# Performance work log

Measured on AMD Instinct MI355X. Metric: run time of the kernel, lower is better.

The kernel has to match this reference:

```python
import jax, jax.numpy as jnp
import numpy as np

ATTEN = 2  # window half-size -> 2*ATTEN+1 = 5 neighbors
B, S, IN, H, MID, OUT = 1024, 100, 100, 128, 32, 2
MAX_LEN = 100
SQRT_H = float(np.sqrt(float(H)))


def _xavier(k, i, o):
    return jax.random.normal(k, (i, o), jnp.float32) * np.sqrt(2.0 / (i + o))


def _positional_encoding():
    pos = np.arange(MAX_LEN, dtype=np.float32)[:, None]
    div = np.exp(np.arange(0, H, 2, dtype=np.float32) * (-np.log(10000.0) / H))
    pe = np.zeros((MAX_LEN, H), np.float32)
    pe[:, 0::2] = np.sin(pos * div)
    pe[:, 1::2] = np.cos(pos * div)
    return jnp.asarray(pe[None])  # (1, MAX_LEN, H)


def setup_inputs() -> dict:
    key = jax.random.key(0)
    ks = jax.random.split(key, 7)
    return {
        "x": jax.random.normal(ks[0], (B, S, IN), jnp.float32),
        "W1": _xavier(ks[1], IN, H),
        "b1": jnp.zeros((1, 1, H), jnp.float32),
        "Wq": _xavier(ks[2], H, H),
        "Wk": _xavier(ks[3], H, H),
        "Wv": _xavier(ks[4], H, H),
        "bv": jnp.zeros((1, 1, H), jnp.float32),
        "W2": _xavier(ks[5], H, MID),
        "b2": jnp.zeros((1, 1, MID), jnp.float32),
        "W3": _xavier(ks[6], MID, OUT),
        "b3": jnp.zeros((1, 1, OUT), jnp.float32),
        "pe": _positional_encoding(),
    }


def reference(x, W1, b1, Wq, Wk, Wv, bv, W2, b2, W3, b3, pe):
    seq_len = x.shape[1]
    h = jax.nn.relu(x @ W1 + b1) + pe[:, :seq_len, :]  # (B,S,H)
    # zero-pad seq dim by ATTEN on each side; torch pad+roll+stack+slice is
    # equivalent to gathering window offsets +2,+1,0,-1,-2 (in that order)
    padded = jnp.pad(h, ((0, 0), (ATTEN, ATTEN), (0, 0)))
    x_nei = jnp.stack(
        [padded[:, ATTEN - k: ATTEN - k + seq_len, :] for k in range(-ATTEN, ATTEN + 1)],
        axis=2,
    )  # (B,S,5,H); index m corresponds to neighbor x[i + ATTEN - m]
    q = h @ Wq                      # (B,S,H)
    keys = x_nei @ Wk               # (B,S,5,H)
    vals = x_nei @ Wv + bv          # (B,S,5,H)
    scores = jnp.einsum("bsh,bswh->bsw", q, keys) / SQRT_H
    w = jax.nn.softmax(scores, axis=-1)  # (B,S,5)
    context = jnp.einsum("bsw,bswh->bsh", w, vals)
    output = jax.nn.relu(context @ W2 + b2) @ W3 + b3  # (B,S,OUT)
    return output, w[:, :, None, :]  # weights shaped (B,S,1,5) like torch
```

## Files before the change

### kernel.cpp

```cpp
#include <hip/hip_runtime.h>
#include <hip/hip_bf16.h>

#define B_ 1024
#define S_ 100
#define IN_ 100
#define H_ 128
#define MID_ 32
#define OUT_ 2
#define P_ (B_ * S_)
#define RSQRT_H 0.08838834764831845f
#define LSTR 136
#define MROWS 100

typedef __attribute__((ext_vector_type(8))) short short8;
typedef __attribute__((ext_vector_type(4))) short short4v;
typedef __attribute__((ext_vector_type(4))) float float4v;

__device__ __forceinline__ float bf2f(ushort u) {
    union { unsigned u; float f; } c; c.u = ((unsigned)u) << 16; return c.f;
}
__device__ __forceinline__ ushort f2bf(float x) {
    union { float f; unsigned u; } c; c.f = x;
    unsigned r = c.u + 0x7FFFu + ((c.u >> 16) & 1u);
    return (ushort)(r >> 16);
}

__global__ __launch_bounds__(256) void prep_kernel(
    const float* __restrict__ W1, const float* __restrict__ Wv,
    const float* __restrict__ W2, const float* __restrict__ Wq,
    const float* __restrict__ Wk,
    ushort* __restrict__ W1T, ushort* __restrict__ WvT,
    ushort* __restrict__ W2T, ushort* __restrict__ WqkT) {
    int tid = threadIdx.x;
    if (blockIdx.x < 144) {
        int g = blockIdx.x * 256 + tid;
        if (g < 16384) {
            int n = g >> 7, k = g & 127;
            W1T[g] = (k < IN_) ? f2bf(W1[k * H_ + n]) : (ushort)0;
        } else if (g < 32768) {
            int e = g - 16384; int n = e >> 7, k = e & 127;
            WvT[e] = f2bf(Wv[k * H_ + n]);
        } else {
            int e = g - 32768; int n = e >> 7, k = e & 127;
            W2T[e] = f2bf(W2[k * MID_ + n]);
        }
    } else {
        __shared__ float sq[32][132];
        __shared__ float sk[32][132];
        int bid = blockIdx.x - 144;
        int n0 = (bid >> 2) * 32, k0 = (bid & 3) * 32;
        for (int i = tid; i < 32 * 32; i += 256) {
            int r = i >> 5, c4 = (i & 31) * 4;
            float4 a = *(const float4*)(Wq + (k0 + r) * H_ + c4);
            float4 b = *(const float4*)(Wk + (n0 + r) * H_ + c4);
            sq[r][c4] = a.x; sq[r][c4 + 1] = a.y; sq[r][c4 + 2] = a.z; sq[r][c4 + 3] = a.w;
            sk[r][c4] = b.x; sk[r][c4 + 1] = b.y; sk[r][c4 + 2] = b.z; sk[r][c4 + 3] = b.w;
        }
        __syncthreads();
        for (int i = tid; i < 1024; i += 256) {
            int kk = i & 31, nn = i >> 5;
            float a0 = 0.f, a1 = 0.f, a2 = 0.f, a3 = 0.f;
#pragma unroll
            for (int j = 0; j < 128; j += 4) {
                a0 += sq[kk][j + 0] * sk[nn][j + 0];
                a1 += sq[kk][j + 1] * sk[nn][j + 1];
                a2 += sq[kk][j + 2] * sk[nn][j + 2];
                a3 += sq[kk][j + 3] * sk[nn][j + 3];
            }
            WqkT[(n0 + nn) * 128 + (k0 + kk)] = f2bf((a0 + a1) + (a2 + a3));
        }
    }
}

template <int EPI>
__device__ __forceinline__ void mm_stage(const ushort* __restrict__ A_lds,
                                         const ushort* __restrict__ WT,
                                         ushort* __restrict__ C_lds,
                                         int wave, int lane,
                                         const float* __restrict__ bias,
                                         const float* __restrict__ pe) {
    int l15 = lane & 15, quad = lane >> 4;
    int n = wave * 16 + l15;
    short8 bfrag[4];
#pragma unroll
    for (int ks = 0; ks < 4; ++ks)
        bfrag[ks] = *(const short8*)(WT + n * 128 + ks * 32 + quad * 8);
    float biasv = 0.f;
    if (EPI != 0) biasv = bias[n];
#pragma unroll
    for (int mt = 0; mt < 7; ++mt) {
        int m0 = (mt < 6) ? mt * 16 : 84;
        short8 afrag[4];
#pragma unroll
        for (int ks = 0; ks < 4; ++ks)
            afrag[ks] = *(const short8*)(A_lds + (m0 + l15) * LSTR + ks * 32 + quad * 8);
        float4v acc = {0.f, 0.f, 0.f, 0.f};
#pragma unroll
        for (int ks = 0; ks < 4; ++ks)
            acc = __builtin_amdgcn_mfma_f32_16x16x32_bf16(afrag[ks], bfrag[ks], acc, 0, 0, 0);
#pragma unroll
        for (int i = 0; i < 4; ++i) {
            int row = m0 + quad * 4 + i;
            float v = acc[i];
            if (EPI == 1) v = fmaxf(v + biasv, 0.f) + pe[row * H_ + n];
            else if (EPI == 2) v = v + biasv;
            C_lds[row * LSTR + n] = f2bf(v);
        }
    }
}

__global__ __launch_bounds__(512, 4) void fused_kernel(
    const float* __restrict__ x, const ushort* __restrict__ W1T,
    const ushort* __restrict__ WqkT, const ushort* __restrict__ WvT,
    const ushort* __restrict__ W2T,
    const float* __restrict__ b1, const float* __restrict__ bv,
    const float* __restrict__ b2, const float* __restrict__ W3,
    const float* __restrict__ b3, const float* __restrict__ pe,
    float* __restrict__ out, float* __restrict__ wout) {
    __shared__ ushort klds[MROWS * LSTR];
    __shared__ ushort xh[MROWS * LSTR];
    int tid = threadIdx.x, wave = tid >> 6, lane = tid & 63;
    int b = blockIdx.x;
    const float* xb = x + (size_t)b * (S_ * IN_);

    for (int i = tid; i < 2500; i += 512) {
        float4 v = ((const float4*)xb)[i];
        int m = i / 25, k4 = (i - m * 25) * 4;
        short4v s;
        s[0] = (short)f2bf(v.x); s[1] = (short)f2bf(v.y);
        s[2] = (short)f2bf(v.z); s[3] = (short)f2bf(v.w);
        *(short4v*)(klds + m * LSTR + k4) = s;
    }
    for (int i = tid; i < S_ * 28; i += 512) {
        int r = i / 28, c = i - r * 28;
        klds[r * LSTR + 100 + c] = 0;
    }
    __syncthreads();
    mm_stage<1>(klds, W1T, xh, wave, lane, b1, pe);
    __syncthreads();
    mm_stage<0>(xh, WqkT, klds, wave, lane, nullptr, nullptr);
    __syncthreads();
    if (tid < 4 * S_) {
        int r = tid >> 2, q = tid & 3;
        const ushort* kqr = klds + r * LSTR + q * 32;
        float kqf[32];
#pragma unroll
        for (int c = 0; c < 4; ++c) {
            short8 v = *(const short8*)(kqr + c * 8);
#pragma unroll
            for (int j = 0; j < 8; ++j) kqf[c * 8 + j] = bf2f((ushort)v[j]);
        }
        float sc[5];
#pragma unroll
        for (int m = 0; m < 5; ++m) {
            int nr = r + 2 - m;
            float p = 0.f;
            if (nr >= 0 && nr < S_) {
                const ushort* hr = xh + nr * LSTR + q * 32;
#pragma unroll
                for (int c = 0; c < 4; ++c) {
                    short8 v = *(const short8*)(hr + c * 8);
#pragma unroll
                    for (int j = 0; j < 8; ++j) p += bf2f((ushort)v[j]) * kqf[c * 8 + j];
                }
            }
            sc[m] = p;
        }
#pragma unroll
        for (int m = 0; m < 5; ++m) {
            sc[m] += __shfl_xor(sc[m], 1);
            sc[m] += __shfl_xor(sc[m], 2);
            sc[m] *= RSQRT_H;
        }
        float mx = sc[0];
#pragma unroll
        for (int m = 1; m < 5; ++m) mx = fmaxf(mx, sc[m]);
        float e[5], ss = 0.f;
#pragma unroll
        for (int m = 0; m < 5; ++m) { e[m] = expf(sc[m] - mx); ss += e[m]; }
        float inv = 1.f / ss;
        float w5[5];
#pragma unroll
        for (int m = 0; m < 5; ++m) w5[m] = e[m] * inv;
        if (q == 0) {
            float* wp = wout + (size_t)b * (S_ * 5) + r * 5;
#pragma unroll
            for (int m = 0; m < 5; ++m) wp[m] = w5[m];
        }
        float acc[32];
#pragma unroll
        for (int c = 0; c < 32; ++c) acc[c] = 0.f;
#pragma unroll
        for (int m = 0; m < 5; ++m) {
            int nr = r + 2 - m;
            if (nr < 0 || nr >= S_) continue;
            float wm = w5[m];
            const ushort* hr = xh + nr * LSTR + q * 32;
#pragma unroll
            for (int c = 0; c < 4; ++c) {
                short8 v = *(const short8*)(hr + c * 8);
#pragma unroll
                for (int j = 0; j < 8; ++j) acc[c * 8 + j] += wm * bf2f((ushort)v[j]);
            }
        }
        ushort* op = klds + r * LSTR + q * 32;
#pragma unroll
        for (int c = 0; c < 4; ++c) {
            short8 v;
#pragma unroll
            for (int j = 0; j < 8; ++j) v[j] = (short)f2bf(acc[c * 8 + j]);
            *(short8*)(op + c * 8) = v;
        }
    }
    __syncthreads();
    mm_stage<2>(klds, WvT, xh, wave, lane, bv, nullptr);
    __syncthreads();
    {
        int l15 = lane & 15, quad = lane >> 4;
        for (int t = wave; t < 14; t += 8) {
            int mt = t >> 1, nt = t & 1;
            int m0 = (mt < 6) ? mt * 16 : 84;
            short8 bfrag[4];
#pragma unroll
            for (int ks = 0; ks < 4; ++ks)
                bfrag[ks] = *(const short8*)(W2T + (nt * 16 + l15) * 128 + ks * 32 + quad * 8);
            float biasv = b2[nt * 16 + l15];
            short8 afrag[4];
#pragma unroll
            for (int ks = 0; ks < 4; ++ks)
                afrag[ks] = *(const short8*)(xh + (m0 + l15) * LSTR + ks * 32 + quad * 8);
            float4v acc = {0.f, 0.f, 0.f, 0.f};
#pragma unroll
            for (int ks = 0; ks < 4; ++ks)
                acc = __builtin_amdgcn_mfma_f32_16x16x32_bf16(afrag[ks], bfrag[ks], acc, 0, 0, 0);
#pragma unroll
            for (int i = 0; i < 4; ++i) {
                int row = m0 + quad * 4 + i;
                klds[row * LSTR + nt * 16 + l15] = f2bf(fmaxf(acc[i] + biasv, 0.f));
            }
        }
    }
    __syncthreads();
    if (tid < S_) {
        int r = tid;
        float o0 = b3[0], o1 = b3[1];
#pragma unroll
        for (int k = 0; k < MID_; ++k) {
            float mv = bf2f(klds[r * LSTR + k]);
            o0 += mv * W3[k * 2];
            o1 += mv * W3[k * 2 + 1];
        }
        float* op = out + (size_t)b * (S_ * OUT_) + r * OUT_;
        op[0] = o0; op[1] = o1;
    }
}

extern "C" void kernel_launch(void* const* d_in, const int* in_sizes, int n_in,
                              void* d_out, int out_size, void* d_ws, size_t ws_size,
                              hipStream_t stream) {
    const float* x  = (const float*)d_in[0];
    const float* W1 = (const float*)d_in[1];
    const float* b1 = (const float*)d_in[2];
    const float* Wq = (const float*)d_in[3];
    const float* Wk = (const float*)d_in[4];
    const float* Wv = (const float*)d_in[5];
    const float* bv = (const float*)d_in[6];
    const float* W2 = (const float*)d_in[7];
    const float* b2 = (const float*)d_in[8];
    const float* W3 = (const float*)d_in[9];
    const float* b3 = (const float*)d_in[10];
    const float* pe = (const float*)d_in[11];

    float* out  = (float*)d_out;
    float* wout = out + (size_t)P_ * OUT_;

    ushort* W1T  = (ushort*)d_ws;
    ushort* WqkT = W1T + 16384;
    ushort* WvT  = WqkT + 16384;
    ushort* W2T  = WvT + 16384;

    prep_kernel<<<160, 256, 0, stream>>>(W1, Wv, W2, Wq, Wk, W1T, WvT, W2T, WqkT);
    fused_kernel<<<B_, 512, 0, stream>>>(x, W1T, WqkT, WvT, W2T,
                                         b1, bv, b2, W3, b3, pe, out, wout);
}
```

Measured before the change: 135.3 us.

## Move local attention scores and context onto MFMA via banded GEMMs

```diff
diff --git a/kernel.cpp b/kernel.cpp
--- a/kernel.cpp
+++ b/kernel.cpp
@@ -10,7 +10,11 @@
 #define P_ (B_ * S_)
 #define RSQRT_H 0.08838834764831845f
 #define LSTR 136
-#define MROWS 100
+#define HSTR 136
+
+#define R1_OFF 13600
+#define R2_OFF 27200
+#define POOL_SHORTS (27200 + 17408)
 
 typedef __attribute__((ext_vector_type(8))) short short8;
 typedef __attribute__((ext_vector_type(4))) short short4v;
@@ -23,6 +27,24 @@
     union { float f; unsigned u; } c; c.f = x;
     unsigned r = c.u + 0x7FFFu + ((c.u >> 16) & 1u);
     return (ushort)(r >> 16);
+}
+
+__device__ const int BAND_M0[19] = {0,0,16,16,16,32,32,32,48,48,48,64,64,64,80,80,80,84,84};
+__device__ const int BAND_N0[19] = {0,16,0,16,32,16,32,48,32,48,64,48,64,80,64,80,84,80,84};
+
+__device__ __forceinline__ float4v gemm_task(const ushort* A, int astr,
+                                             const ushort* Bt, int bstr,
+                                             int m0, int n0, int ks0, int ks1,
+                                             int l15, int quad) {
+    float4v acc = {0.f, 0.f, 0.f, 0.f};
+    const ushort* ap = A + (m0 + l15) * astr + quad * 8;
+    const ushort* bp = Bt + (n0 + l15) * bstr + quad * 8;
+    for (int ks = ks0; ks <= ks1; ++ks) {
+        short8 a = *(const short8*)(ap + ks * 32);
+        short8 b = *(const short8*)(bp + ks * 32);
+        acc = __builtin_amdgcn_mfma_f32_16x16x32_bf16(a, b, acc, 0, 0, 0);
+    }
+    return acc;
 }
 
 __global__ __launch_bounds__(256) void prep_kernel(
@@ -72,44 +94,7 @@
     }
 }
 
-template <int EPI>
-__device__ __forceinline__ void mm_stage(const ushort* __restrict__ A_lds,
-                                         const ushort* __restrict__ WT,
-                                         ushort* __restrict__ C_lds,
-                                         int wave, int lane,
-                                         const float* __restrict__ bias,
-                                         const float* __restrict__ pe) {
-    int l15 = lane & 15, quad = lane >> 4;
-    int n = wave * 16 + l15;
-    short8 bfrag[4];
-#pragma unroll
-    for (int ks = 0; ks < 4; ++ks)
-        bfrag[ks] = *(const short8*)(WT + n * 128 + ks * 32 + quad * 8);
-    float biasv = 0.f;
-    if (EPI != 0) biasv = bias[n];
-#pragma unroll
-    for (int mt = 0; mt < 7; ++mt) {
-        int m0 = (mt < 6) ? mt * 16 : 84;
-        short8 afrag[4];
-#pragma unroll
-        for (int ks = 0; ks < 4; ++ks)
-            afrag[ks] = *(const short8*)(A_lds + (m0 + l15) * LSTR + ks * 32 + quad * 8);
-        float4v acc = {0.f, 0.f, 0.f, 0.f};
-#pragma unroll
-        for (int ks = 0; ks < 4; ++ks)
-            acc = __builtin_amdgcn_mfma_f32_16x16x32_bf16(afrag[ks], bfrag[ks], acc, 0, 0, 0);
-#pragma unroll
-        for (int i = 0; i < 4; ++i) {
-            int row = m0 + quad * 4 + i;
-            float v = acc[i];
-            if (EPI == 1) v = fmaxf(v + biasv, 0.f) + pe[row * H_ + n];
-            else if (EPI == 2) v = v + biasv;
-            C_lds[row * LSTR + n] = f2bf(v);
-        }
-    }
-}
-
-__global__ __launch_bounds__(512, 4) void fused_kernel(
+__global__ __launch_bounds__(1024, 4) void fused_kernel(
     const float* __restrict__ x, const ushort* __restrict__ W1T,
     const ushort* __restrict__ WqkT, const ushort* __restrict__ WvT,
     const ushort* __restrict__ W2T,
@@ -117,138 +102,151 @@
     const float* __restrict__ b2, const float* __restrict__ W3,
     const float* __restrict__ b3, const float* __restrict__ pe,
     float* __restrict__ out, float* __restrict__ wout) {
-    __shared__ ushort klds[MROWS * LSTR];
-    __shared__ ushort xh[MROWS * LSTR];
+    __shared__ __align__(16) ushort pool[POOL_SHORTS];
+    ushort* R0 = pool;
+    ushort* R1 = pool + R1_OFF;
+    ushort* R2 = pool + R2_OFF;
+    float* scf = (float*)R2;
+
     int tid = threadIdx.x, wave = tid >> 6, lane = tid & 63;
+    int l15 = lane & 15, quad = lane >> 4;
     int b = blockIdx.x;
     const float* xb = x + (size_t)b * (S_ * IN_);
 
-    for (int i = tid; i < 2500; i += 512) {
+    for (int i = tid; i < 2500; i += 1024) {
         float4 v = ((const float4*)xb)[i];
         int m = i / 25, k4 = (i - m * 25) * 4;
         short4v s;
         s[0] = (short)f2bf(v.x); s[1] = (short)f2bf(v.y);
         s[2] = (short)f2bf(v.z); s[3] = (short)f2bf(v.w);
-        *(short4v*)(klds + m * LSTR + k4) = s;
-    }
-    for (int i = tid; i < S_ * 28; i += 512) {
+        *(short4v*)(R0 + m * LSTR + k4) = s;
+    }
+    for (int i = tid; i < S_ * 28; i += 1024) {
         int r = i / 28, c = i - r * 28;
-        klds[r * LSTR + 100 + c] = 0;
-    }
-    __syncthreads();
-    mm_stage<1>(klds, W1T, xh, wave, lane, b1, pe);
-    __syncthreads();
-    mm_stage<0>(xh, WqkT, klds, wave, lane, nullptr, nullptr);
-    __syncthreads();
-    if (tid < 4 * S_) {
-        int r = tid >> 2, q = tid & 3;
-        const ushort* kqr = klds + r * LSTR + q * 32;
-        float kqf[32];
-#pragma unroll
-        for (int c = 0; c < 4; ++c) {
-            short8 v = *(const short8*)(kqr + c * 8);
-#pragma unroll
-            for (int j = 0; j < 8; ++j) kqf[c * 8 + j] = bf2f((ushort)v[j]);
-        }
-        float sc[5];
+        R0[r * LSTR + 100 + c] = 0;
+    }
+    if (tid < 800) scf[tid] = 0.f;
+    __syncthreads();
+
+    for (int t = wave; t < 56; t += 16) {
+        int mt = t >> 3, nt = t & 7;
+        int m0 = (mt < 6) ? mt * 16 : 84, n0 = nt * 16;
+        float4v acc = gemm_task(R0, LSTR, W1T, 128, m0, n0, 0, 3, l15, quad);
+        int n = n0 + l15;
+        float bb = b1[n];
+#pragma unroll
+        for (int i = 0; i < 4; ++i) {
+            int row = m0 + quad * 4 + i;
+            R1[row * LSTR + n] = f2bf(fmaxf(acc[i] + bb, 0.f) + pe[row * H_ + n]);
+        }
+    }
+    __syncthreads();
+
+    for (int t = wave; t < 56; t += 16) {
+        int mt = t >> 3, nt = t & 7;
+        int m0 = (mt < 6) ? mt * 16 : 84, n0 = nt * 16;
+        float4v acc = gemm_task(R1, LSTR, WqkT, 128, m0, n0, 0, 3, l15, quad);
+        int n = n0 + l15;
+#pragma unroll
+        for (int i = 0; i < 4; ++i)
+            R0[(m0 + quad * 4 + i) * LSTR + n] = f2bf(acc[i]);
+    }
+    __syncthreads();
+
+    for (int t = wave; t < 19; t += 16) {
+        int m0 = BAND_M0[t], n0 = BAND_N0[t];
+        float4v acc = gemm_task(R0, LSTR, R1, LSTR, m0, n0, 0, 3, l15, quad);
+        int col = n0 + l15;
+#pragma unroll
+        for (int i = 0; i < 4; ++i) {
+            int row = m0 + quad * 4 + i;
+            int m = row - col + 2;
+            if ((unsigned)m <= 4u) scf[row * 8 + m] = acc[i];
+        }
+    }
+    __syncthreads();
+
+    {
+        short8 z = {0, 0, 0, 0, 0, 0, 0, 0};
+        for (int i = tid; i < 1600; i += 1024)
+            *(short8*)(R0 + (i >> 4) * LSTR + (i & 15) * 8) = z;
+    }
+    __syncthreads();
+    if (tid < S_) {
+        int r = tid;
+        float sc5[5];
+#pragma unroll
+        for (int m = 0; m < 5; ++m) sc5[m] = scf[r * 8 + m] * RSQRT_H;
+        float mx = fmaxf(fmaxf(fmaxf(sc5[0], sc5[1]), fmaxf(sc5[2], sc5[3])), sc5[4]);
+        float e[5], ss = 0.f;
+#pragma unroll
+        for (int m = 0; m < 5; ++m) { e[m] = expf(sc5[m] - mx); ss += e[m]; }
+        float inv = 1.f / ss;
+        float* wp = wout + (size_t)b * (S_ * 5) + r * 5;
 #pragma unroll
         for (int m = 0; m < 5; ++m) {
-            int nr = r + 2 - m;
-            float p = 0.f;
-            if (nr >= 0 && nr < S_) {
-                const ushort* hr = xh + nr * LSTR + q * 32;
-#pragma unroll
-                for (int c = 0; c < 4; ++c) {
-                    short8 v = *(const short8*)(hr + c * 8);
-#pragma unroll
-                    for (int j = 0; j < 8; ++j) p += bf2f((ushort)v[j]) * kqf[c * 8 + j];
-                }
-            }
-            sc[m] = p;
-        }
-#pragma unroll
-        for (int m = 0; m < 5; ++m) {
-            sc[m] += __shfl_xor(sc[m], 1);
-            sc[m] += __shfl_xor(sc[m], 2);
-            sc[m] *= RSQRT_H;
-        }
-        float mx = sc[0];
-#pragma unroll
-        for (int m = 1; m < 5; ++m) mx = fmaxf(mx, sc[m]);
-        float e[5], ss = 0.f;
-#pragma unroll
-        for (int m = 0; m < 5; ++m) { e[m] = expf(sc[m] - mx); ss += e[m]; }
-        float inv = 1.f / ss;
-        float w5[5];
-#pragma unroll
-        for (int m = 0; m < 5; ++m) w5[m] = e[m] * inv;
-        if (q == 0) {
-            float* wp = wout + (size_t)b * (S_ * 5) + r * 5;
-#pragma unroll
-            for (int m = 0; m < 5; ++m) wp[m] = w5[m];
-        }
-        float acc[32];
-#pragma unroll
-        for (int c = 0; c < 32; ++c) acc[c] = 0.f;
-#pragma unroll
-        for (int m = 0; m < 5; ++m) {
-            int nr = r + 2 - m;
-            if (nr < 0 || nr >= S_) continue;
-            float wm = w5[m];
-            const ushort* hr = xh + nr * LSTR + q * 32;
-#pragma unroll
-            for (int c = 0; c < 4; ++c) {
-                short8 v = *(const short8*)(hr + c * 8);
-#pragma unroll
-                for (int j = 0; j < 8; ++j) acc[c * 8 + j] += wm * bf2f((ushort)v[j]);
-            }
-        }
-        ushort* op = klds + r * LSTR + q * 32;
-#pragma unroll
-        for (int c = 0; c < 4; ++c) {
-            short8 v;
-#pragma unroll
-            for (int j = 0; j < 8; ++j) v[j] = (short)f2bf(acc[c * 8 + j]);
-            *(short8*)(op + c * 8) = v;
-        }
-    }
-    __syncthreads();
-    mm_stage<2>(klds, WvT, xh, wave, lane, bv, nullptr);
-    __syncthreads();
-    {
-        int l15 = lane & 15, quad = lane >> 4;
-        for (int t = wave; t < 14; t += 8) {
-            int mt = t >> 1, nt = t & 1;
-            int m0 = (mt < 6) ? mt * 16 : 84;
-            short8 bfrag[4];
-#pragma unroll
-            for (int ks = 0; ks < 4; ++ks)
-                bfrag[ks] = *(const short8*)(W2T + (nt * 16 + l15) * 128 + ks * 32 + quad * 8);
-            float biasv = b2[nt * 16 + l15];
-            short8 afrag[4];
-#pragma unroll
-            for (int ks = 0; ks < 4; ++ks)
-                afrag[ks] = *(const short8*)(xh + (m0 + l15) * LSTR + ks * 32 + quad * 8);
-            float4v acc = {0.f, 0.f, 0.f, 0.f};
-#pragma unroll
-            for (int ks = 0; ks < 4; ++ks)
-                acc = __builtin_amdgcn_mfma_f32_16x16x32_bf16(afrag[ks], bfrag[ks], acc, 0, 0, 0);
-#pragma unroll
-            for (int i = 0; i < 4; ++i) {
-                int row = m0 + quad * 4 + i;
-                klds[row * LSTR + nt * 16 + l15] = f2bf(fmaxf(acc[i] + biasv, 0.f));
-            }
-        }
-    }
-    __syncthreads();
+            float w = e[m] * inv;
+            wp[m] = w;
+            int c = r + 2 - m;
+            if (0 <= c && c < S_) R0[r * LSTR + c] = f2bf(w);
+        }
+    }
+    __syncthreads();
+
+    for (int t = wave; t < 56; t += 16) {
+        int nt = t >> 3, mt = t & 7;
+        int m0 = mt * 16, n0 = (nt < 6) ? nt * 16 : 84;
+        float4v acc = gemm_task(WvT, 128, R1, LSTR, m0, n0, 0, 3, l15, quad);
+        int c = n0 + l15;
+#pragma unroll
+        for (int i = 0; i < 4; ++i)
+            R2[(m0 + quad * 4 + i) * HSTR + c] = f2bf(acc[i]);
+    }
+    for (int i = tid; i < 128 * 28; i += 1024) {
+        int r = i / 28, c = i - r * 28;
+        R2[r * HSTR + 100 + c] = 0;
+    }
+    __syncthreads();
+
+    for (int t = wave; t < 56; t += 16) {
+        int mt = t >> 3, nt = t & 7;
+        int m0 = (mt < 6) ? mt * 16 : 84, n0 = nt * 16;
+        int ks0 = (m0 - 2) >> 5; if (ks0 < 0) ks0 = 0;
+        int ks1 = (m0 + 19) >> 5; if (ks1 > 3) ks1 = 3;
+        float4v acc = gemm_task(R0, LSTR, R2, HSTR, m0, n0, ks0, ks1, l15, quad);
+        int n = n0 + l15;
+        float bb = bv[n];
+#pragma unroll
+        for (int i = 0; i < 4; ++i)
+            R1[(m0 + quad * 4 + i) * LSTR + n] = f2bf(acc[i] + bb);
+    }
+    __syncthreads();
+
+    for (int t = wave; t < 14; t += 16) {
+        int mt = t >> 1, nt = t & 1;
+        int m0 = (mt < 6) ? mt * 16 : 84, n0 = nt * 16;
+        float4v acc = gemm_task(R1, LSTR, W2T, 128, m0, n0, 0, 3, l15, quad);
+        int n = n0 + l15;
+        float bb = b2[n];
+#pragma unroll
+        for (int i = 0; i < 4; ++i)
+            R0[(m0 + quad * 4 + i) * LSTR + n] = f2bf(fmaxf(acc[i] + bb, 0.f));
+    }
+    __syncthreads();
+
     if (tid < S_) {
         int r = tid;
         float o0 = b3[0], o1 = b3[1];
 #pragma unroll
-        for (int k = 0; k < MID_; ++k) {
-            float mv = bf2f(klds[r * LSTR + k]);
-            o0 += mv * W3[k * 2];
-            o1 += mv * W3[k * 2 + 1];
+        for (int c8 = 0; c8 < 4; ++c8) {
+            short8 v = *(const short8*)(R0 + r * LSTR + c8 * 8);
+#pragma unroll
+            for (int j = 0; j < 8; ++j) {
+                float mv = bf2f((ushort)v[j]);
+                int k = c8 * 8 + j;
+                o0 += mv * W3[k * 2];
+                o1 += mv * W3[k * 2 + 1];
+            }
         }
         float* op = out + (size_t)b * (S_ * OUT_) + r * OUT_;
         op[0] = o0; op[1] = o1;
@@ -280,6 +278,6 @@
     ushort* W2T  = WvT + 16384;
 
     prep_kernel<<<160, 256, 0, stream>>>(W1, Wv, W2, Wq, Wk, W1T, WvT, W2T, WqkT);
-    fused_kernel<<<B_, 512, 0, stream>>>(x, W1T, WqkT, WvT, W2T,
-                                         b1, bv, b2, W3, b3, pe, out, wout);
-}
+    fused_kernel<<<B_, 1024, 0, stream>>>(x, W1T, WqkT, WvT, W2T,
+                                          b1, bv, b2, W3, b3, pe, out, wout);
+}
```

Result: slower. 204.9 us (+51.4%).

## Compute windowed attention scores with banded MFMA tiles instead of scalar dot products

Applied to the files above, without the earlier changes.

```diff
diff --git a/kernel.cpp b/kernel.cpp
--- a/kernel.cpp
+++ b/kernel.cpp
@@ -10,7 +10,6 @@
 #define P_ (B_ * S_)
 #define RSQRT_H 0.08838834764831845f
 #define LSTR 136
-#define MROWS 100
 
 typedef __attribute__((ext_vector_type(8))) short short8;
 typedef __attribute__((ext_vector_type(4))) short short4v;
@@ -24,6 +23,9 @@
     unsigned r = c.u + 0x7FFFu + ((c.u >> 16) & 1u);
     return (ushort)(r >> 16);
 }
+
+__device__ const int BAND_M0[19] = {0,0,16,16,16,32,32,32,48,48,48,64,64,64,80,80,80,84,84};
+__device__ const int BAND_N0[19] = {0,16,0,16,32,16,32,48,32,48,64,48,64,80,64,80,84,80,84};
 
 __global__ __launch_bounds__(256) void prep_kernel(
     const float* __restrict__ W1, const float* __restrict__ Wv,
@@ -117,9 +119,12 @@
     const float* __restrict__ b2, const float* __restrict__ W3,
     const float* __restrict__ b3, const float* __restrict__ pe,
     float* __restrict__ out, float* __restrict__ wout) {
-    __shared__ ushort klds[MROWS * LSTR];
-    __shared__ ushort xh[MROWS * LSTR];
+    __shared__ __align__(16) ushort R0[S_ * LSTR];
+    __shared__ __align__(16) ushort R1[S_ * LSTR];
+    __shared__ float scf[S_ * 8];
+
     int tid = threadIdx.x, wave = tid >> 6, lane = tid & 63;
+    int l15 = lane & 15, quad = lane >> 4;
     int b = blockIdx.x;
     const float* xb = x + (size_t)b * (S_ * IN_);
 
@@ -129,55 +134,51 @@
         short4v s;
         s[0] = (short)f2bf(v.x); s[1] = (short)f2bf(v.y);
         s[2] = (short)f2bf(v.z); s[3] = (short)f2bf(v.w);
-        *(short4v*)(klds + m * LSTR + k4) = s;
+        *(short4v*)(R0 + m * LSTR + k4) = s;
     }
     for (int i = tid; i < S_ * 28; i += 512) {
         int r = i / 28, c = i - r * 28;
-        klds[r * LSTR + 100 + c] = 0;
-    }
-    __syncthreads();
-    mm_stage<1>(klds, W1T, xh, wave, lane, b1, pe);
-    __syncthreads();
-    mm_stage<0>(xh, WqkT, klds, wave, lane, nullptr, nullptr);
-    __syncthreads();
+        R0[r * LSTR + 100 + c] = 0;
+    }
+    for (int i = tid; i < S_ * 8; i += 512) scf[i] = 0.f;
+    __syncthreads();
+
+    mm_stage<1>(R0, W1T, R1, wave, lane, b1, pe);
+    __syncthreads();
+
+    mm_stage<0>(R1, WqkT, R0, wave, lane, nullptr, nullptr);
+    __syncthreads();
+
+    for (int t = wave; t < 19; t += 8) {
+        int m0 = BAND_M0[t], n0 = BAND_N0[t];
+        const ushort* ap = R0 + (m0 + l15) * LSTR + quad * 8;
+        const ushort* bp = R1 + (n0 + l15) * LSTR + quad * 8;
+        float4v acc = {0.f, 0.f, 0.f, 0.f};
+#pragma unroll
+        for (int ks = 0; ks < 4; ++ks) {
+            short8 a = *(const short8*)(ap + ks * 32);
+            short8 bb = *(const short8*)(bp + ks * 32);
+            acc = __builtin_amdgcn_mfma_f32_16x16x32_bf16(a, bb, acc, 0, 0, 0);
+        }
+        int col = n0 + l15;
+#pragma unroll
+        for (int i = 0; i < 4; ++i) {
+            int row = m0 + quad * 4 + i;
+            int m = row - col + 2;
+            if ((unsigned)m <= 4u) scf[row * 8 + m] = acc[i];
+        }
+    }
+    __syncthreads();
+
     if (tid < 4 * S_) {
         int r = tid >> 2, q = tid & 3;
-        const ushort* kqr = klds + r * LSTR + q * 32;
-        float kqf[32];
-#pragma unroll
-        for (int c = 0; c < 4; ++c) {
-            short8 v = *(const short8*)(kqr + c * 8);
-#pragma unroll
-            for (int j = 0; j < 8; ++j) kqf[c * 8 + j] = bf2f((ushort)v[j]);
-        }
-        float sc[5];
-#pragma unroll
-        for (int m = 0; m < 5; ++m) {
-            int nr = r + 2 - m;
-            float p = 0.f;
-            if (nr >= 0 && nr < S_) {
-                const ushort* hr = xh + nr * LSTR + q * 32;
-#pragma unroll
-                for (int c = 0; c < 4; ++c) {
-                    short8 v = *(const short8*)(hr + c * 8);
-#pragma unroll
-                    for (int j = 0; j < 8; ++j) p += bf2f((ushort)v[j]) * kqf[c * 8 + j];
-                }
-            }
-            sc[m] = p;
-        }
-#pragma unroll
-        for (int m = 0; m < 5; ++m) {
-            sc[m] += __shfl_xor(sc[m], 1);
-            sc[m] += __shfl_xor(sc[m], 2);
-            sc[m] *= RSQRT_H;
-        }
-        float mx = sc[0];
-#pragma unroll
-        for (int m = 1; m < 5; ++m) mx = fmaxf(mx, sc[m]);
+        float sc5[5];
+#pragma unroll
+        for (int m = 0; m < 5; ++m) sc5[m] = scf[r * 8 + m] * RSQRT_H;
+        float mx = fmaxf(fmaxf(fmaxf(sc5[0], sc5[1]), fmaxf(sc5[2], sc5[3])), sc5[4]);
         float e[5], ss = 0.f;
 #pragma unroll
-        for (int m = 0; m < 5; ++m) { e[m] = expf(sc[m] - mx); ss += e[m]; }
+        for (int m = 0; m < 5; ++m) { e[m] = expf(sc5[m] - mx); ss += e[m]; }
         float inv = 1.f / ss;
         float w5[5];
 #pragma unroll
@@ -195,7 +196,7 @@
             int nr = r + 2 - m;
             if (nr < 0 || nr >= S_) continue;
             float wm = w5[m];
-            const ushort* hr = xh + nr * LSTR + q * 32;
+            const ushort* hr = R1 + nr * LSTR + q * 32;
 #pragma unroll
             for (int c = 0; c < 4; ++c) {
                 short8 v = *(const short8*)(hr + c * 8);
@@ -203,7 +204,7 @@
                 for (int j = 0; j < 8; ++j) acc[c * 8 + j] += wm * bf2f((ushort)v[j]);
             }
         }
-        ushort* op = klds + r * LSTR + q * 32;
+        ushort* op = R0 + r * LSTR + q * 32;
 #pragma unroll
         for (int c = 0; c < 4; ++c) {
             short8 v;
@@ -213,42 +214,45 @@
         }
     }
     __syncthreads();
-    mm_stage<2>(klds, WvT, xh, wave, lane, bv, nullptr);
-    __syncthreads();
-    {
-        int l15 = lane & 15, quad = lane >> 4;
-        for (int t = wave; t < 14; t += 8) {
-            int mt = t >> 1, nt = t & 1;
-            int m0 = (mt < 6) ? mt * 16 : 84;
-            short8 bfrag[4];
-#pragma unroll
-            for (int ks = 0; ks < 4; ++ks)
-                bfrag[ks] = *(const short8*)(W2T + (nt * 16 + l15) * 128 + ks * 32 + quad * 8);
-            float biasv = b2[nt * 16 + l15];
-            short8 afrag[4];
-#pragma unroll
-            for (int ks = 0; ks < 4; ++ks)
-                afrag[ks] = *(const short8*)(xh + (m0 + l15) * LSTR + ks * 32 + quad * 8);
-            float4v acc = {0.f, 0.f, 0.f, 0.f};
-#pragma unroll
-            for (int ks = 0; ks < 4; ++ks)
-                acc = __builtin_amdgcn_mfma_f32_16x16x32_bf16(afrag[ks], bfrag[ks], acc, 0, 0, 0);
-#pragma unroll
-            for (int i = 0; i < 4; ++i) {
-                int row = m0 + quad * 4 + i;
-                klds[row * LSTR + nt * 16 + l15] = f2bf(fmaxf(acc[i] + biasv, 0.f));
-            }
-        }
-    }
-    __syncthreads();
+
+    mm_stage<2>(R0, WvT, R1, wave, lane, bv, nullptr);
+    __syncthreads();
+
+    for (int t = wave; t < 14; t += 8) {
+        int mt = t >> 1, nt = t & 1;
+        int m0 = (mt < 6) ? mt * 16 : 84, n0 = nt * 16;
+        short8 bfrag[4], afrag[4];
+#pragma unroll
+        for (int ks = 0; ks < 4; ++ks) {
+            bfrag[ks] = *(const short8*)(W2T + (n0 + l15) * 128 + ks * 32 + quad * 8);
+            afrag[ks] = *(const short8*)(R1 + (m0 + l15) * LSTR + ks * 32 + quad * 8);
+        }
+        float biasv = b2[n0 + l15];
+        float4v acc = {0.f, 0.f, 0.f, 0.f};
+#pragma unroll
+        for (int ks = 0; ks < 4; ++ks)
+            acc = __builtin_amdgcn_mfma_f32_16x16x32_bf16(afrag[ks], bfrag[ks], acc, 0, 0, 0);
+#pragma unroll
+        for (int i = 0; i < 4; ++i) {
+            int row = m0 + quad * 4 + i;
+            R0[row * LSTR + n0 + l15] = f2bf(fmaxf(acc[i] + biasv, 0.f));
+        }
+    }
+    __syncthreads();
+
     if (tid < S_) {
         int r = tid;
         float o0 = b3[0], o1 = b3[1];
 #pragma unroll
-        for (int k = 0; k < MID_; ++k) {
-            float mv = bf2f(klds[r * LSTR + k]);
-            o0 += mv * W3[k * 2];
-            o1 += mv * W3[k * 2 + 1];
+        for (int c8 = 0; c8 < 4; ++c8) {
+            short8 v = *(const short8*)(R0 + r * LSTR + c8 * 8);
+#pragma unroll
+            for (int j = 0; j < 8; ++j) {
+                float mv = bf2f((ushort)v[j]);
+                int k = c8 * 8 + j;
+                o0 += mv * W3[k * 2];
+                o1 += mv * W3[k * 2 + 1];
+            }
         }
         float* op = out + (size_t)b * (S_ * OUT_) + r * OUT_;
         op[0] = o0; op[1] = o1;
```

Measured after the change: 135.9 us. About the same (+0.5%).
